# Performance work log

Measured on AMD Instinct MI355X. Metric: run time of the kernel, lower is better.

## Reference

```python
import jax, jax.numpy as jnp
import numpy as np

TOL = 5               # proximity_tolerance
PROX_REWARD = 2.0     # proximity_reward
FAR_PENALTY = 1.5     # far_penalty
CLASS_WEIGHTS = np.array([0.1, 5.0, 5.0], dtype=np.float32)


def setup_inputs() -> dict:
    key = jax.random.key(0)
    k1, k2 = jax.random.split(key)
    B, S, C = 512, 16384, 3
    logits = jax.random.normal(k1, (B, S, C), dtype=jnp.float32)
    labels = jax.random.randint(k2, (B, S), 0, 3)
    return {"logits": logits, "labels": labels}


def _window_any(mask_bool, tol):
    # True at position p iff mask is True anywhere in [p-tol, p+tol] (clipped at edges).
    pooled = jax.lax.reduce_window(
        mask_bool.astype(jnp.float32), 0.0, jax.lax.max,
        window_dimensions=(1, 2 * tol + 1), window_strides=(1, 1),
        padding=[(0, 0), (tol, tol)])
    return pooled > 0.5


def reference(logits, labels):
    B, S, C = logits.shape
    w = jnp.asarray(CLASS_WEIGHTS)

    valid = labels != -100                      # [B,S]
    labels_safe = jnp.where(valid, labels, 0)

    # Weighted cross-entropy, reduction='none' (weight applied per-element, ignore_index -> 0)
    logp = jax.nn.log_softmax(logits, axis=-1)  # [B,S,C]
    picked = jnp.take_along_axis(logp, labels_safe[..., None], axis=-1)[..., 0]
    base_loss = jnp.where(valid, -w[labels_safe] * picked, 0.0)  # [B,S]

    predictions = jnp.argmax(logits, axis=-1)   # [B,S] int
    pred_sw = predictions >= 1                  # predicted switch positions
    true_sw = labels >= 1                       # true switch positions (-100 < 1 so excluded)

    pred_near = _window_any(pred_sw, TOL)       # any predicted switch within +/-TOL
    true_near = _window_any(true_sw, TOL)       # any true switch within +/-TOL
    has_true = jnp.any(true_sw, axis=1, keepdims=True)  # far-penalty only applies if batch row has true switches

    reward_mask = (true_sw & pred_near).astype(jnp.float32)
    penalty_mask = (pred_sw & (~true_near) & has_true).astype(jnp.float32)
    additive = -PROX_REWARD * reward_mask + FAR_PENALTY * penalty_mask

    vm = valid.astype(jnp.float32)
    return ((base_loss + additive) * vm).sum() / vm.sum()
```

## Files before the change

kernel.cpp:

```cpp
#include <hip/hip_runtime.h>
#include <hip/hip_bf16.h>


#define TOL 5
#define BLOCK 256
#define SROW 16384
#define GPRW (SROW / 64)
#define CHUNK 1024
#define NITER (SROW / CHUNK)

typedef unsigned long long u64;

__global__ __launch_bounds__(BLOCK) void k1_row(
    const float* __restrict__ logits, const int* __restrict__ labels,
    float* __restrict__ row_sum, int* __restrict__ row_cnt)
{
    __shared__ float lds_l[CHUNK * 3];
    __shared__ int   lds_lab[CHUNK];
    __shared__ u64 pm_s[GPRW], tm_s[GPRW], vm_s[GPRW];
    __shared__ float wb[4];
    __shared__ int wv[4], rs[4], ps[4], hs[4];

    const int tid = threadIdx.x;
    const int wave = tid >> 6;
    const int row = blockIdx.x;
    const long long rowbase = (long long)row * SROW;

    const float4* gl4 = (const float4*)(logits + rowbase * 3);
    const int4*   gi4 = (const int4*)(labels + rowbase);

    float4 pf0 = gl4[tid], pf1 = gl4[tid + BLOCK], pf2 = gl4[tid + 2 * BLOCK];
    int4   pi  = gi4[tid];

    float bsum = 0.f;
    int   vcnt = 0;

    for (int it = 0; it < NITER; ++it) {
        ((float4*)lds_l)[tid]             = pf0;
        ((float4*)lds_l)[tid + BLOCK]     = pf1;
        ((float4*)lds_l)[tid + 2 * BLOCK] = pf2;
        ((int4*)lds_lab)[tid]             = pi;
        __syncthreads();

        if (it + 1 < NITER) {
            const float4* g = gl4 + (long long)(it + 1) * (CHUNK * 3 / 4);
            pf0 = g[tid]; pf1 = g[tid + BLOCK]; pf2 = g[tid + 2 * BLOCK];
            pi  = gi4[(long long)(it + 1) * (CHUNK / 4) + tid];
        }

#pragma unroll
        for (int q = 0; q < CHUNK / BLOCK; ++q) {
            const int pos = q * BLOCK + tid;
            const float l0 = lds_l[3 * pos + 0];
            const float l1 = lds_l[3 * pos + 1];
            const float l2 = lds_l[3 * pos + 2];
            const int lab = lds_lab[pos];

            const bool valid = (lab != -100);
            const int ls = valid ? lab : 0;

            const float mx = fmaxf(l0, fmaxf(l1, l2));
            const float se = __expf(l0 - mx) + __expf(l1 - mx) + __expf(l2 - mx);
            const float lse = mx + __logf(se);
            const float lpick = (ls == 0 ? l0 : (ls == 1 ? l1 : l2)) - lse;
            const float w = (ls == 0) ? 0.1f : 5.0f;
            bsum += valid ? (-w * lpick) : 0.f;
            vcnt += valid ? 1 : 0;

            const bool psw = fmaxf(l1, l2) > l0;
            const bool tsw = (lab >= 1);

            const u64 pm = __ballot(psw);
            const u64 tm = __ballot(tsw);
            const u64 vm = __ballot(valid);
            if ((tid & 63) == 0) {
                const int g = it * (CHUNK / 64) + q * (BLOCK / 64) + wave;
                pm_s[g] = pm; tm_s[g] = tm; vm_s[g] = vm;
            }
        }
        __syncthreads();
    }

    const u64 pm = pm_s[tid], tm = tm_s[tid], vm = vm_s[tid];
    const u64 pp = (tid > 0)        ? pm_s[tid - 1] : 0ULL;
    const u64 pn = (tid < GPRW - 1) ? pm_s[tid + 1] : 0ULL;
    const u64 tp = (tid > 0)        ? tm_s[tid - 1] : 0ULL;
    const u64 tn = (tid < GPRW - 1) ? tm_s[tid + 1] : 0ULL;

    u64 pnear = pm, tnear = tm;
#pragma unroll
    for (int k = 1; k <= TOL; ++k) {
        pnear |= (pm << k) | (pm >> k) | (pp >> (64 - k)) | (pn << (64 - k));
        tnear |= (tm << k) | (tm >> k) | (tp >> (64 - k)) | (tn << (64 - k));
    }

    int reward  = __popcll(tm & pnear);
    int penalty = __popcll(pm & ~tnear & vm);
    int ht = (tm != 0ULL) ? 1 : 0;

#pragma unroll
    for (int off = 32; off; off >>= 1) {
        bsum    += __shfl_down(bsum, off);
        vcnt    += __shfl_down(vcnt, off);
        reward  += __shfl_down(reward, off);
        penalty += __shfl_down(penalty, off);
        ht      |= __shfl_down(ht, off);
    }
    if ((tid & 63) == 0) { wb[wave] = bsum; wv[wave] = vcnt; rs[wave] = reward; ps[wave] = penalty; hs[wave] = ht; }
    __syncthreads();
    if (tid == 0) {
        float S = 0.f; int C = 0, R = 0, P = 0, H = 0;
#pragma unroll
        for (int i = 0; i < 4; ++i) { S += wb[i]; C += wv[i]; R += rs[i]; P += ps[i]; H |= hs[i]; }
        row_sum[row] = S - 2.0f * (float)R + (H ? 1.5f * (float)P : 0.0f);
        row_cnt[row] = C;
    }
}

__global__ __launch_bounds__(BLOCK) void k2_final(
    const float* __restrict__ row_sum, const int* __restrict__ row_cnt,
    int nrows, float* __restrict__ out)
{
    const int t = threadIdx.x;
    double s = 0.0;
    long long c = 0;
    for (int i = t; i < nrows; i += BLOCK) { s += (double)row_sum[i]; c += (long long)row_cnt[i]; }

#pragma unroll
    for (int off = 32; off; off >>= 1) {
        s += __shfl_down(s, off);
        c += __shfl_down(c, off);
    }
    __shared__ double ss[4];
    __shared__ long long cs[4];
    const int wave = t >> 6;
    if ((t & 63) == 0) { ss[wave] = s; cs[wave] = c; }
    __syncthreads();
    if (t == 0) {
        double S = 0.0; long long C = 0;
#pragma unroll
        for (int i = 0; i < 4; ++i) { S += ss[i]; C += cs[i]; }
        out[0] = (float)(S / (double)C);
    }
}

extern "C" void kernel_launch(void* const* d_in, const int* in_sizes, int n_in,
                              void* d_out, int out_size, void* d_ws, size_t ws_size,
                              hipStream_t stream) {
    const float* logits = (const float*)d_in[0];
    const int*   labels = (const int*)d_in[1];
    float* out = (float*)d_out;

    const long long BS = in_sizes[1];
    const int B = (int)(BS / SROW);

    char* ws = (char*)d_ws;
    float* row_sum = (float*)ws;
    int*   row_cnt = (int*)(row_sum + B);

    k1_row<<<B, BLOCK, 0, stream>>>(logits, labels, row_sum, row_cnt);
    k2_final<<<1, BLOCK, 0, stream>>>(row_sum, row_cnt, B, out);
}
```

Measured before the change: 174.5 us.

## Fuse final reduction via last-block atomic and drop LDS staging for direct loads

Merges the per-row kernel and the final reduction kernel into one launch: each block bumps an atomic counter after writing its row result, and the last block to finish does the global reduction. A memset resets the counter before each launch. The LDS-staged, double-buffered float4 loads are replaced by direct strided scalar loads from global memory, with a 4x unroll and only one barrier. This removes a kernel launch and the per-chunk barriers, but the 12-byte-stride scalar loads may coalesce worse than the old vectorized loads, and the row count is now hardcoded.

```diff
diff --git a/kernel.cpp b/kernel.cpp
--- a/kernel.cpp
+++ b/kernel.cpp
@@ -5,87 +5,68 @@
 #define TOL 5
 #define BLOCK 256
 #define SROW 16384
-#define GPRW (SROW / 64)
-#define CHUNK 1024
-#define NITER (SROW / CHUNK)
+#define NROWS 512
 
 typedef unsigned long long u64;
+typedef unsigned int u32;
 
-__global__ __launch_bounds__(BLOCK) void k1_row(
+__global__ __launch_bounds__(BLOCK) void k_all(
     const float* __restrict__ logits, const int* __restrict__ labels,
-    float* __restrict__ row_sum, int* __restrict__ row_cnt)
+    float* __restrict__ row_sum, int* __restrict__ row_cnt,
+    u32* __restrict__ done, float* __restrict__ out)
 {
-    __shared__ float lds_l[CHUNK * 3];
-    __shared__ int   lds_lab[CHUNK];
-    __shared__ u64 pm_s[GPRW], tm_s[GPRW], vm_s[GPRW];
+    __shared__ u64 pm_s[BLOCK], tm_s[BLOCK], vm_s[BLOCK];
     __shared__ float wb[4];
     __shared__ int wv[4], rs[4], ps[4], hs[4];
+    __shared__ int islast;
 
     const int tid = threadIdx.x;
     const int wave = tid >> 6;
     const int row = blockIdx.x;
     const long long rowbase = (long long)row * SROW;
-
-    const float4* gl4 = (const float4*)(logits + rowbase * 3);
-    const int4*   gi4 = (const int4*)(labels + rowbase);
-
-    float4 pf0 = gl4[tid], pf1 = gl4[tid + BLOCK], pf2 = gl4[tid + 2 * BLOCK];
-    int4   pi  = gi4[tid];
+    const float* lg = logits + 3 * rowbase;
+    const int*   lb = labels + rowbase;
 
     float bsum = 0.f;
     int   vcnt = 0;
 
-    for (int it = 0; it < NITER; ++it) {
-        ((float4*)lds_l)[tid]             = pf0;
-        ((float4*)lds_l)[tid + BLOCK]     = pf1;
-        ((float4*)lds_l)[tid + 2 * BLOCK] = pf2;
-        ((int4*)lds_lab)[tid]             = pi;
-        __syncthreads();
+#pragma unroll 4
+    for (int i = 0; i < SROW / BLOCK; ++i) {
+        const int pos = i * BLOCK + tid;
+        const float l0 = lg[3 * pos + 0];
+        const float l1 = lg[3 * pos + 1];
+        const float l2 = lg[3 * pos + 2];
+        const int lab = lb[pos];
 
-        if (it + 1 < NITER) {
-            const float4* g = gl4 + (long long)(it + 1) * (CHUNK * 3 / 4);
-            pf0 = g[tid]; pf1 = g[tid + BLOCK]; pf2 = g[tid + 2 * BLOCK];
-            pi  = gi4[(long long)(it + 1) * (CHUNK / 4) + tid];
+        const bool valid = (lab != -100);
+        const int ls = valid ? lab : 0;
+
+        const float mx = fmaxf(l0, fmaxf(l1, l2));
+        const float se = __expf(l0 - mx) + __expf(l1 - mx) + __expf(l2 - mx);
+        const float lse = mx + __logf(se);
+        const float lpick = (ls == 0 ? l0 : (ls == 1 ? l1 : l2)) - lse;
+        const float w = (ls == 0) ? 0.1f : 5.0f;
+        bsum += valid ? (-w * lpick) : 0.f;
+        vcnt += valid ? 1 : 0;
+
+        const bool psw = fmaxf(l1, l2) > l0;
+        const bool tsw = (lab >= 1);
+
+        const u64 pmm = __ballot(psw);
+        const u64 tmm = __ballot(tsw);
+        const u64 vmm = __ballot(valid);
+        if ((tid & 63) == 0) {
+            const int g = i * 4 + wave;
+            pm_s[g] = pmm; tm_s[g] = tmm; vm_s[g] = vmm;
         }
-
-#pragma unroll
-        for (int q = 0; q < CHUNK / BLOCK; ++q) {
-            const int pos = q * BLOCK + tid;
-            const float l0 = lds_l[3 * pos + 0];
-            const float l1 = lds_l[3 * pos + 1];
-            const float l2 = lds_l[3 * pos + 2];
-            const int lab = lds_lab[pos];
-
-            const bool valid = (lab != -100);
-            const int ls = valid ? lab : 0;
-
-            const float mx = fmaxf(l0, fmaxf(l1, l2));
-            const float se = __expf(l0 - mx) + __expf(l1 - mx) + __expf(l2 - mx);
-            const float lse = mx + __logf(se);
-            const float lpick = (ls == 0 ? l0 : (ls == 1 ? l1 : l2)) - lse;
-            const float w = (ls == 0) ? 0.1f : 5.0f;
-            bsum += valid ? (-w * lpick) : 0.f;
-            vcnt += valid ? 1 : 0;
-
-            const bool psw = fmaxf(l1, l2) > l0;
-            const bool tsw = (lab >= 1);
-
-            const u64 pm = __ballot(psw);
-            const u64 tm = __ballot(tsw);
-            const u64 vm = __ballot(valid);
-            if ((tid & 63) == 0) {
-                const int g = it * (CHUNK / 64) + q * (BLOCK / 64) + wave;
-                pm_s[g] = pm; tm_s[g] = tm; vm_s[g] = vm;
-            }
-        }
-        __syncthreads();
     }
+    __syncthreads();
 
     const u64 pm = pm_s[tid], tm = tm_s[tid], vm = vm_s[tid];
-    const u64 pp = (tid > 0)        ? pm_s[tid - 1] : 0ULL;
-    const u64 pn = (tid < GPRW - 1) ? pm_s[tid + 1] : 0ULL;
-    const u64 tp = (tid > 0)        ? tm_s[tid - 1] : 0ULL;
-    const u64 tn = (tid < GPRW - 1) ? tm_s[tid + 1] : 0ULL;
+    const u64 pp = (tid > 0)         ? pm_s[tid - 1] : 0ULL;
+    const u64 pn = (tid < BLOCK - 1) ? pm_s[tid + 1] : 0ULL;
+    const u64 tp = (tid > 0)         ? tm_s[tid - 1] : 0ULL;
+    const u64 tn = (tid < BLOCK - 1) ? tm_s[tid + 1] : 0ULL;
 
     u64 pnear = pm, tnear = tm;
 #pragma unroll
@@ -108,39 +89,41 @@
     }
     if ((tid & 63) == 0) { wb[wave] = bsum; wv[wave] = vcnt; rs[wave] = reward; ps[wave] = penalty; hs[wave] = ht; }
     __syncthreads();
+
     if (tid == 0) {
         float S = 0.f; int C = 0, R = 0, P = 0, H = 0;
 #pragma unroll
         for (int i = 0; i < 4; ++i) { S += wb[i]; C += wv[i]; R += rs[i]; P += ps[i]; H |= hs[i]; }
         row_sum[row] = S - 2.0f * (float)R + (H ? 1.5f * (float)P : 0.0f);
         row_cnt[row] = C;
+        __threadfence();
+        const u32 prev = atomicAdd(done, 1u);
+        islast = (prev == (u32)(NROWS - 1)) ? 1 : 0;
     }
-}
+    __syncthreads();
 
-__global__ __launch_bounds__(BLOCK) void k2_final(
-    const float* __restrict__ row_sum, const int* __restrict__ row_cnt,
-    int nrows, float* __restrict__ out)
-{
-    const int t = threadIdx.x;
-    double s = 0.0;
-    long long c = 0;
-    for (int i = t; i < nrows; i += BLOCK) { s += (double)row_sum[i]; c += (long long)row_cnt[i]; }
-
+    if (islast) {
+        __threadfence();
+        double s = 0.0; long long c = 0;
+        for (int i = tid; i < NROWS; i += BLOCK) {
+            s += (double)row_sum[i];
+            c += (long long)row_cnt[i];
+        }
 #pragma unroll
-    for (int off = 32; off; off >>= 1) {
-        s += __shfl_down(s, off);
-        c += __shfl_down(c, off);
-    }
-    __shared__ double ss[4];
-    __shared__ long long cs[4];
-    const int wave = t >> 6;
-    if ((t & 63) == 0) { ss[wave] = s; cs[wave] = c; }
-    __syncthreads();
-    if (t == 0) {
-        double S = 0.0; long long C = 0;
+        for (int off = 32; off; off >>= 1) {
+            s += __shfl_down(s, off);
+            c += __shfl_down(c, off);
+        }
+        __shared__ double ss[4];
+        __shared__ long long cs[4];
+        if ((tid & 63) == 0) { ss[wave] = s; cs[wave] = c; }
+        __syncthreads();
+        if (tid == 0) {
+            double S = 0.0; long long C = 0;
 #pragma unroll
-        for (int i = 0; i < 4; ++i) { S += ss[i]; C += cs[i]; }
-        out[0] = (float)(S / (double)C);
+            for (int i = 0; i < 4; ++i) { S += ss[i]; C += cs[i]; }
+            out[0] = (float)(S / (double)C);
+        }
     }
 }
 
@@ -151,13 +134,11 @@
     const int*   labels = (const int*)d_in[1];
     float* out = (float*)d_out;
 
-    const long long BS = in_sizes[1];
-    const int B = (int)(BS / SROW);
-
     char* ws = (char*)d_ws;
     float* row_sum = (float*)ws;
-    int*   row_cnt = (int*)(row_sum + B);
+    int*   row_cnt = (int*)(row_sum + NROWS);
+    u32*   done    = (u32*)(row_cnt + NROWS);
 
-    k1_row<<<B, BLOCK, 0, stream>>>(logits, labels, row_sum, row_cnt);
-    k2_final<<<1, BLOCK, 0, stream>>>(row_sum, row_cnt, B, out);
+    hipMemsetAsync(done, 0, sizeof(u32), stream);
+    k_all<<<NROWS, BLOCK, 0, stream>>>(logits, labels, row_sum, row_cnt, done, out);
 }
```

Result: slower. 201.7 us (+15.6%).
